# Performance work log

Measured on AMD Instinct MI355X. Metric: run time of the kernel, lower is better.

## Reference

```python
import jax, jax.numpy as jnp
import numpy as np

D_MODEL = 1024
N_HEADS = 16
D_K = D_MODEL // N_HEADS
SEQ = 2048
BATCH = 2
THETA = 10000.0


def apply_rope(x, positions, theta):
    # x: [..., h, s, d_k], positions: [s]
    d_k = x.shape[-1]
    inv_freq = 1.0 / (theta ** (jnp.arange(0, d_k, 2, dtype=jnp.float32) / d_k))  # [d_k/2]
    ang = positions.astype(jnp.float32)[:, None] * inv_freq[None, :]  # [s, d_k/2]
    cos, sin = jnp.cos(ang), jnp.sin(ang)
    xe, xo = x[..., 0::2], x[..., 1::2]
    re = xe * cos - xo * sin
    ro = xe * sin + xo * cos
    return jnp.stack([re, ro], axis=-1).reshape(x.shape)


def setup_inputs() -> dict:
    key = jax.random.key(0)
    ks = jax.random.split(key, 7)
    f = lambda k, s: jax.random.normal(k, s, dtype=jnp.float32)
    return {
        "Q": f(ks[0], (BATCH, SEQ, D_MODEL)),
        "K": f(ks[1], (BATCH, SEQ, D_MODEL)),
        "V": f(ks[2], (BATCH, SEQ, D_MODEL)),
        "w_q": f(ks[3], (D_MODEL, D_MODEL)) * 0.02,
        "w_k": f(ks[4], (D_MODEL, D_MODEL)) * 0.02,
        "w_v": f(ks[5], (D_MODEL, D_MODEL)) * 0.02,
        "w_o": f(ks[6], (D_MODEL, D_MODEL)) * 0.02,
        "mask": jnp.tril(jnp.ones((SEQ, SEQ), dtype=bool)),
        "token_positions": jnp.arange(SEQ, dtype=jnp.int32),
    }


def reference(Q, K, V, w_q, w_k, w_v, w_o, mask, token_positions):
    h, d_k = N_HEADS, D_K
    # projections: weight is [h*d_k, d_model], applied as x @ W^T
    def proj(x, w):
        y = jnp.einsum('bsd,ed->bse', x, w)
        b, s, _ = y.shape
        return y.reshape(b, s, h, d_k).transpose(0, 2, 1, 3)  # [b,h,s,d_k]
    q = proj(Q, w_q)
    k = proj(K, w_k)
    v = proj(V, w_v)
    q = apply_rope(q, token_positions, THETA)
    k = apply_rope(k, token_positions, THETA)
    scores = jnp.einsum('bhqd,bhkd->bhqk', q, k) / jnp.sqrt(jnp.float32(d_k))
    scores = jnp.where(mask, scores, -jnp.inf)
    attn = jax.nn.softmax(scores, axis=-1)
    out = jnp.einsum('bhqk,bhkd->bhqd', attn, v)
    b, _, s, _ = out.shape
    out = out.transpose(0, 2, 1, 3).reshape(b, s, h * d_k)
    return jnp.einsum('bse,de->bsd', out, w_o)
```

## Files before the change

kernel.cpp:

```cpp
#include <hip/hip_runtime.h>

#define SEQ 2048
#define BATCH 2
#define DM 1024
#define NH 16
#define DK 64
#define BH (BATCH*NH)

typedef __attribute__((ext_vector_type(8))) short bf16x8;
typedef __attribute__((ext_vector_type(4))) float f32x4;

__device__ __forceinline__ ushort f2bf(float f) {
  union { float f; unsigned u; } v; v.f = f;
  unsigned r = (v.u + 0x7fffu + ((v.u >> 16) & 1u)) >> 16;
  return (ushort)r;
}
__device__ __forceinline__ float bf2f(ushort h) {
  union { unsigned u; float f; } v; v.u = ((unsigned)h) << 16;
  return v.f;
}
__device__ __forceinline__ unsigned cvtpk(float lo, float hi) {
  unsigned r;
  asm("v_cvt_pk_bf16_f32 %0, %1, %2" : "=v"(r) : "v"(lo), "v"(hi));
  return r;
}

#define WAITV4 asm volatile("s_waitcnt vmcnt(4)" ::: "memory")
#define WAITV3 asm volatile("s_waitcnt vmcnt(3)" ::: "memory")
#define WAITV0 asm volatile("s_waitcnt vmcnt(0)" ::: "memory")
#define WAITL0 asm volatile("s_waitcnt lgkmcnt(0)" ::: "memory")
#define BARR() __builtin_amdgcn_s_barrier()

struct P4 { const float* p0; const float* p1; const float* p2; const float* p3; };
__global__ void k_castN(P4 in, ushort* __restrict__ out, int n4) {
  const float* src = (blockIdx.z == 0) ? in.p0 : (blockIdx.z == 1) ? in.p1
                    : (blockIdx.z == 2) ? in.p2 : in.p3;
  ushort* dst = out + (size_t)blockIdx.z * (size_t)n4 * 4;
  int i = blockIdx.x * blockDim.x + threadIdx.x;
  int st = gridDim.x * blockDim.x;
  for (; i < n4; i += st) {
    float4 v = reinterpret_cast<const float4*>(src)[i];
    ushort4 o;
    o.x = f2bf(v.x); o.y = f2bf(v.y); o.z = f2bf(v.z); o.w = f2bf(v.w);
    reinterpret_cast<ushort4*>(dst)[i] = o;
  }
}

__global__ void k_rope_tab(float* __restrict__ tab) {
  int id = blockIdx.x * blockDim.x + threadIdx.x;
  if (id >= SEQ * 32) return;
  int s = id >> 5, i = id & 31;
  float inv = powf(10000.f, -(float)i / 32.f);
  float ang = (float)s * inv;
  float sn, cs;
  sincosf(ang, &sn, &cs);
  tab[id * 2] = cs;
  tab[id * 2 + 1] = sn;
}

__global__ __launch_bounds__(256) void k_tr_v(const ushort* __restrict__ Y,
                                              ushort* __restrict__ VT) {
  __shared__ ushort tile[64][65];
  const int st = blockIdx.x, bh = blockIdx.y;
  const int b = bh >> 4, h = bh & 15;
  const int d = threadIdx.x & 63, s4 = threadIdx.x >> 6;
#pragma unroll
  for (int p = 0; p < 16; ++p) {
    int sl = p * 4 + s4;
    tile[d][sl] = Y[(size_t)(b * SEQ + st * 64 + sl) * DM + h * 64 + d];
  }
  __syncthreads();
  const int sl = threadIdx.x & 63, d4 = threadIdx.x >> 6;
#pragma unroll
  for (int p = 0; p < 16; ++p) {
    int dl = p * 4 + d4;
    VT[(size_t)bh * DK * SEQ + (size_t)dl * SEQ + st * 64 + sl] = tile[dl][sl];
  }
}

__device__ __forceinline__ void gll16(const void* g, void* l) {
  __builtin_amdgcn_global_load_lds((const __attribute__((address_space(1))) void*)g,
                                   (__attribute__((address_space(3))) void*)l, 16, 0, 0);
}

#define GSTAGE(AD, BD, kk_) do {                                               \
    gll16(A + (size_t)(m0 + w * 16 + lrow) * K + (kk_) + lcol, (void*)((AD) + w * 512));        \
    gll16(A + (size_t)(m0 + 64 + w * 16 + lrow) * K + (kk_) + lcol, (void*)((AD) + 2048 + w * 512)); \
    gll16(Bw + (size_t)(n0 + w * 16 + lrow) * K + (kk_) + lcol, (void*)((BD) + w * 512));       \
    gll16(Bw + (size_t)(n0 + 64 + w * 16 + lrow) * K + (kk_) + lcol, (void*)((BD) + 2048 + w * 512)); \
  } while (0)

#define GCOMP(AS_, BS_) do {                                                   \
    bf16x8 af[4], bfr[4];                                                      \
    _Pragma("unroll")                                                          \
    for (int i = 0; i < 4; ++i)                                                \
      af[i] = *(const bf16x8*)((AS_) + (wr * 64 + i * 16 + l15) * 32 + l4 * 8);\
    _Pragma("unroll")                                                          \
    for (int i = 0; i < 4; ++i)                                                \
      bfr[i] = *(const bf16x8*)((BS_) + (wc * 64 + i * 16 + l15) * 32 + l4 * 8);\
    _Pragma("unroll")                                                          \
    for (int mi = 0; mi < 4; ++mi)                                             \
      _Pragma("unroll")                                                        \
      for (int ni = 0; ni < 4; ++ni)                                           \
        acc[mi][ni] = __builtin_amdgcn_mfma_f32_16x16x32_bf16(af[mi], bfr[ni], acc[mi][ni], 0, 0, 0); \
  } while (0)

__global__ __launch_bounds__(256) void k_gemm_qkv(const ushort* __restrict__ A,
                                                  const ushort* __restrict__ Bw,
                                                  ushort* __restrict__ qT,
                                                  ushort* __restrict__ kT,
                                                  ushort* __restrict__ YV,
                                                  const float* __restrict__ tab,
                                                  float qscale, int M, int N, int K) {
  const int id = blockIdx.x;
  const int mlo = id & 7, nb = (id >> 3) & 7, mhi = (id >> 6) & 3, z = id >> 8;
  const int m0 = (mhi * 8 + mlo) * 128, n0 = nb * 128;
  A += (size_t)z * ((size_t)M * K);
  Bw += (size_t)z * ((size_t)N * K);
  __shared__ ushort As0[128 * 32], Bs0[128 * 32];
  __shared__ ushort As1[128 * 32], Bs1[128 * 32];
  const int tid = threadIdx.x;
  const int w = tid >> 6, lane = tid & 63;
  const int l15 = lane & 15, l4 = lane >> 4;
  const int wr = w >> 1, wc = w & 1;
  const int lrow = lane >> 2, lcol = (lane & 3) * 8;
  f32x4 acc[4][4] = {};
  GSTAGE(As0, Bs0, 0);
  GSTAGE(As1, Bs1, 32);
  for (int kk = 0; kk < K - 64; kk += 64) {
    WAITV4; BARR();
    GCOMP(As0, Bs0);
    WAITL0; BARR();
    GSTAGE(As0, Bs0, kk + 64);
    WAITV4; BARR();
    GCOMP(As1, Bs1);
    WAITL0; BARR();
    if (kk + 96 < K) GSTAGE(As1, Bs1, kk + 96);
  }
  WAITV4; BARR();
  GCOMP(As0, Bs0);
  WAITV0; BARR();
  GCOMP(As1, Bs1);
  if (z == 2) {
#pragma unroll
    for (int mi = 0; mi < 4; ++mi)
#pragma unroll
      for (int ni = 0; ni < 4; ++ni)
#pragma unroll
        for (int r = 0; r < 4; ++r) {
          int row = m0 + wr * 64 + mi * 16 + l4 * 4 + r;
          int col = n0 + wc * 64 + ni * 16 + l15;
          YV[(size_t)row * N + col] = f2bf(acc[mi][ni][r]);
        }
  } else {
    const float scale = (z == 0) ? qscale : 1.0f;
    ushort* T = (z == 0) ? qT : kT;
    const bool odd = (l15 & 1);
#pragma unroll
    for (int mi = 0; mi < 4; ++mi)
#pragma unroll
      for (int ni = 0; ni < 4; ++ni)
#pragma unroll
        for (int r = 0; r < 4; ++r) {
          int row = m0 + wr * 64 + mi * 16 + l4 * 4 + r;
          int col = n0 + wc * 64 + ni * 16 + l15;
          float v = acc[mi][ni][r];
          float pv = __shfl_xor(v, 1);
          int s = row & (SEQ - 1);
          int d = col & 63;
          float2 cs = *(const float2*)(tab + ((size_t)s * 32 + (d >> 1)) * 2);
          float xe = odd ? pv : v, xo = odd ? v : pv;
          float outv = (odd ? (xe * cs.y + xo * cs.x) : (xe * cs.x - xo * cs.y)) * scale;
          int bh = (row >> 11) * 16 + (col >> 6);
          T[((size_t)bh * SEQ + s) * 64 + d] = f2bf(outv);
        }
  }
}

#define FSTAGE(AD, BD, kk_) do {                                               \
    gll16(A + (size_t)(m0 + srow) * K + (kk_) + scol, (void*)((AD) + w * 512));\
    gll16(Bw + (size_t)(n0 + srow) * K + (kk_) + scol, (void*)((BD) + w * 512));\
    gll16(Bw + (size_t)(n0 + 64 + srow) * K + (kk_) + scol, (void*)((BD) + 2048 + w * 512)); \
  } while (0)

#define FCOMP(AS_, BS_) do {                                                   \
    bf16x8 af[2], bfr[4];                                                      \
    _Pragma("unroll")                                                          \
    for (int i = 0; i < 2; ++i)                                                \
      af[i] = *(const bf16x8*)((AS_) + (wr * 32 + i * 16 + l15) * 32 + l4 * 8);\
    _Pragma("unroll")                                                          \
    for (int i = 0; i < 4; ++i)                                                \
      bfr[i] = *(const bf16x8*)((BS_) + (wc * 64 + i * 16 + l15) * 32 + l4 * 8);\
    _Pragma("unroll")                                                          \
    for (int mi = 0; mi < 2; ++mi)                                             \
      _Pragma("unroll")                                                        \
      for (int ni = 0; ni < 4; ++ni)                                           \
        acc[mi][ni] = __builtin_amdgcn_mfma_f32_16x16x32_bf16(af[mi], bfr[ni], acc[mi][ni], 0, 0, 0); \
  } while (0)

__global__ __launch_bounds__(256) void k_gemm_f(const ushort* __restrict__ A,
                                                const ushort* __restrict__ Bw,
                                                float* __restrict__ C, int M, int N, int K) {
  const int id = blockIdx.x;
  const int mlo = id & 7, nb = (id >> 3) & 7, mhi = id >> 6;
  const int m0 = (mhi * 8 + mlo) * 64, n0 = nb * 128;
  __shared__ ushort As0[64 * 32], Bs0[128 * 32];
  __shared__ ushort As1[64 * 32], Bs1[128 * 32];
  const int tid = threadIdx.x;
  const int w = tid >> 6, lane = tid & 63;
  const int l15 = lane & 15, l4 = lane >> 4;
  const int wr = w >> 1, wc = w & 1;
  const int srow = tid >> 2, scol = (tid & 3) * 8;
  f32x4 acc[2][4] = {};
  FSTAGE(As0, Bs0, 0);
  FSTAGE(As1, Bs1, 32);
  for (int kk = 0; kk < K - 64; kk += 64) {
    WAITV3; BARR();
    FCOMP(As0, Bs0);
    WAITL0; BARR();
    FSTAGE(As0, Bs0, kk + 64);
    WAITV3; BARR();
    FCOMP(As1, Bs1);
    WAITL0; BARR();
    if (kk + 96 < K) FSTAGE(As1, Bs1, kk + 96);
  }
  WAITV3; BARR();
  FCOMP(As0, Bs0);
  WAITV0; BARR();
  FCOMP(As1, Bs1);
#pragma unroll
  for (int mi = 0; mi < 2; ++mi)
#pragma unroll
    for (int ni = 0; ni < 4; ++ni)
#pragma unroll
      for (int r = 0; r < 4; ++r) {
        int row = m0 + wr * 32 + mi * 16 + l4 * 4 + r;
        int col = n0 + wc * 64 + ni * 16 + l15;
        C[(size_t)row * N + col] = acc[mi][ni][r];
      }
}

#define STAGE1(DST, src, srcstride) do {                                       \
    _Pragma("unroll")                                                          \
    for (int i_ = 0; i_ < 2; ++i_) {                                           \
      int tt_ = i_ * 256 + tid;                                                \
      int row_ = tt_ >> 3, c_ = (tt_ & 7) ^ (row_ & 7);                        \
      gll16(src + (size_t)row_ * (srcstride) + c_ * 8,                         \
            (void*)((char*)(DST) + (i_ * 256 + w * 64) * 16));                 \
    }                                                                          \
  } while (0)

#define STAGE(KD, VD, kt_) do {                                                \
    const ushort* kb_ = kT + hb + (size_t)(kt_) * 4096;                        \
    const ushort* vb_ = vT + vbase + (size_t)(kt_) * 64;                       \
    STAGE1(KD, kb_, 64);                                                       \
    STAGE1(VD, vb_, SEQ);                                                      \
  } while (0)

#define LDSFRAG(BASE, row_, cidx)                                              \
  (*(const bf16x8*)((const char*)(BASE) + (row_) * 128 + (((cidx) ^ (l15 & 7)) * 16)))

#define SMAXUPD(P, MRUN, LRUN, SO) do {                                        \
    float a0 = fmaxf(fmaxf(P[0][0], P[0][1]), fmaxf(P[0][2], P[0][3]));        \
    float a1 = fmaxf(fmaxf(P[1][0], P[1][1]), fmaxf(P[1][2], P[1][3]));        \
    float a2 = fmaxf(fmaxf(P[2][0], P[2][1]), fmaxf(P[2][2], P[2][3]));        \
    float a3 = fmaxf(fmaxf(P[3][0], P[3][1]), fmaxf(P[3][2], P[3][3]));        \
    float mx = fmaxf(fmaxf(a0, a1), fmaxf(a2, a3));                            \
    mx = fmaxf(mx, __shfl_xor(mx, 16));                                        \
    mx = fmaxf(mx, __shfl_xor(mx, 32));                                        \
    const float mn = fmaxf(MRUN, mx);                                          \
    SO = __builtin_amdgcn_exp2f(MRUN - mn);                                    \
    float rs = 0.f;                                                            \
    _Pragma("unroll")                                                          \
    for (int nf = 0; nf < 4; ++nf) {                                           \
      float e0 = __builtin_amdgcn_exp2f(P[nf][0] - mn);                        \
      float e1 = __builtin_amdgcn_exp2f(P[nf][1] - mn);                        \
      float e2 = __builtin_amdgcn_exp2f(P[nf][2] - mn);                        \
      float e3 = __builtin_amdgcn_exp2f(P[nf][3] - mn);                        \
      P[nf][0] = e0; P[nf][1] = e1; P[nf][2] = e2; P[nf][3] = e3;              \
      rs += (e0 + e1) + (e2 + e3);                                             \
    }                                                                          \
    rs += __shfl_xor(rs, 16);                                                  \
    rs += __shfl_xor(rs, 32);                                                  \
    LRUN = LRUN * SO + rs;                                                     \
    MRUN = mn;                                                                 \
  } while (0)

#define RESCALE(ACC, SO) do {                                                  \
    float soq[4];                                                              \
    _Pragma("unroll")                                                          \
    for (int r = 0; r < 4; ++r) soq[r] = __shfl(SO, l4 * 4 + r);               \
    _Pragma("unroll")                                                          \
    for (int df = 0; df < 4; ++df)                                             \
      _Pragma("unroll")                                                        \
      for (int r = 0; r < 4; ++r) ACC[df][r] *= soq[r];                        \
  } while (0)

#define PWRITE(P, MYP) do {                                                    \
    _Pragma("unroll")                                                          \
    for (int nf = 0; nf < 4; ++nf) {                                           \
      uint2 pk;                                                                \
      pk.x = cvtpk(P[nf][0], P[nf][1]);                                        \
      pk.y = cvtpk(P[nf][2], P[nf][3]);                                        \
      *(uint2*)((MYP) + ((l15 * 128 + nf * 32 + l4 * 8) ^ swz)) = pk;          \
    }                                                                          \
  } while (0)

#define STEP2(KC, VC, KN, VN, kt_, M0, M1, PREF) do {                          \
    if (PREF) { STAGE(KN, VN, (kt_) + 1); }                                    \
    float p0[4][4], p1[4][4];                                                  \
    _Pragma("unroll")                                                          \
    for (int nf = 0; nf < 4; ++nf) {                                           \
      bf16x8 k0_ = LDSFRAG(KC, nf * 16 + l15, l4);                             \
      bf16x8 k1_ = LDSFRAG(KC, nf * 16 + l15, l4 + 4);                         \
      if (M0 >= 0) {                                                           \
        f32x4 z = {0.f, 0.f, 0.f, 0.f};                                        \
        z = __builtin_amdgcn_mfma_f32_16x16x32_bf16(k0_, qb00, z, 0, 0, 0);    \
        z = __builtin_amdgcn_mfma_f32_16x16x32_bf16(k1_, qb01, z, 0, 0, 0);    \
        _Pragma("unroll")                                                      \
        for (int r = 0; r < 4; ++r) {                                          \
          float sc = z[r];                                                     \
          if (M0 == 1 && (nf * 16 + l4 * 4 + r) > (w * 16 + l15)) sc = -INFINITY; \
          p0[nf][r] = sc;                                                      \
        }                                                                      \
      }                                                                        \
      {                                                                        \
        f32x4 z = {0.f, 0.f, 0.f, 0.f};                                        \
        z = __builtin_amdgcn_mfma_f32_16x16x32_bf16(k0_, qb10, z, 0, 0, 0);    \
        z = __builtin_amdgcn_mfma_f32_16x16x32_bf16(k1_, qb11, z, 0, 0, 0);    \
        _Pragma("unroll")                                                      \
        for (int r = 0; r < 4; ++r) {                                          \
          float sc = z[r];                                                     \
          if (M1 == 1 && (nf * 16 + l4 * 4 + r) > (w * 16 + l15)) sc = -INFINITY; \
          p1[nf][r] = sc;                                                      \
        }                                                                      \
      }                                                                        \
    }                                                                          \
    float so0_, so1_;                                                          \
    if (M0 >= 0) { SMAXUPD(p0, mrun0, lrun0, so0_); RESCALE(acc0, so0_); PWRITE(p0, myP0); } \
    SMAXUPD(p1, mrun1, lrun1, so1_); RESCALE(acc1, so1_); PWRITE(p1, myP1);    \
    bf16x8 pa00, pa01, pa10, pa11;                                             \
    if (M0 >= 0) {                                                             \
      pa00 = *(const bf16x8*)(myP0 + ((l15 * 128 + l4 * 16) ^ swz));           \
      pa01 = *(const bf16x8*)(myP0 + ((l15 * 128 + 64 + l4 * 16) ^ swz));      \
    }                                                                          \
    pa10 = *(const bf16x8*)(myP1 + ((l15 * 128 + l4 * 16) ^ swz));             \
    pa11 = *(const bf16x8*)(myP1 + ((l15 * 128 + 64 + l4 * 16) ^ swz));        \
    _Pragma("unroll")                                                          \
    for (int df = 0; df < 4; ++df) {                                           \
      bf16x8 v0_ = LDSFRAG(VC, df * 16 + l15, l4);                             \
      bf16x8 v1_ = LDSFRAG(VC, df * 16 + l15, l4 + 4);                         \
      if (M0 >= 0) {                                                           \
        acc0[df] = __builtin_amdgcn_mfma_f32_16x16x32_bf16(pa00, v0_, acc0[df], 0, 0, 0); \
        acc0[df] = __builtin_amdgcn_mfma_f32_16x16x32_bf16(pa01, v1_, acc0[df], 0, 0, 0); \
      }                                                                        \
      acc1[df] = __builtin_amdgcn_mfma_f32_16x16x32_bf16(pa10, v0_, acc1[df], 0, 0, 0); \
      acc1[df] = __builtin_amdgcn_mfma_f32_16x16x32_bf16(pa11, v1_, acc1[df], 0, 0, 0); \
    }                                                                          \
    __syncthreads();                                                           \
  } while (0)

__global__ __launch_bounds__(256, 3) void k_flash(const ushort* __restrict__ qT,
                                                  const ushort* __restrict__ kT,
                                                  const ushort* __restrict__ vT,
                                                  ushort* __restrict__ AO) {
  __shared__ ushort Ks[2][64 * 64];
  __shared__ ushort Vs[2][64 * 64];
  __shared__ char Plds[4 * 4096];
  const int l = blockIdx.x;
  const int bh = (l & 7) * 4 + ((l >> 3) & 3);
  const int qt = (SEQ / 128 - 1) - (l >> 5);
  const int tid = threadIdx.x, w = tid >> 6, lane = tid & 63;
  const int l15 = lane & 15, l4 = lane >> 4;
  const size_t hb = (size_t)bh * SEQ * DK;
  const size_t vbase = (size_t)bh * DK * SEQ;
  const int qrow0 = qt * 128 + w * 16;
  const int qrow1 = qrow0 + 64;
  const bf16x8 qb00 = *(const bf16x8*)(qT + hb + (size_t)(qrow0 + l15) * 64 + l4 * 8);
  const bf16x8 qb01 = *(const bf16x8*)(qT + hb + (size_t)(qrow0 + l15) * 64 + 32 + l4 * 8);
  const bf16x8 qb10 = *(const bf16x8*)(qT + hb + (size_t)(qrow1 + l15) * 64 + l4 * 8);
  const bf16x8 qb11 = *(const bf16x8*)(qT + hb + (size_t)(qrow1 + l15) * 64 + 32 + l4 * 8);
  f32x4 acc0[4] = {}, acc1[4] = {};
  float mrun0 = -INFINITY, lrun0 = 0.f, mrun1 = -INFINITY, lrun1 = 0.f;
  char* myP0 = (char*)Plds + w * 4096;
  char* myP1 = myP0 + 2048;
  const int swz = (l15 & 7) << 4;
  ushort* kc = &Ks[0][0]; ushort* vc = &Vs[0][0];
  ushort* kn = &Ks[1][0]; ushort* vn = &Vs[1][0];
  STAGE(kc, vc, 0);
  __syncthreads();
  for (int kt = 0; kt < 2 * qt; ++kt) {
    STEP2(kc, vc, kn, vn, kt, 0, 0, true);
    ushort* t;
    t = kc; kc = kn; kn = t;
    t = vc; vc = vn; vn = t;
  }
  STEP2(kc, vc, kn, vn, 2 * qt, 1, 0, true);
  {
    ushort* t;
    t = kc; kc = kn; kn = t;
    t = vc; vc = vn; vn = t;
  }
  STEP2(kc, vc, kn, vn, 2 * qt + 1, -1, 1, false);
  const int b = bh >> 4, h = bh & 15;
  float lq0[4], lq1[4];
#pragma unroll
  for (int r = 0; r < 4; ++r) {
    lq0[r] = __shfl(lrun0, l4 * 4 + r);
    lq1[r] = __shfl(lrun1, l4 * 4 + r);
  }
#pragma unroll
  for (int r = 0; r < 4; ++r) {
    float inv0 = 1.f / lq0[r], inv1 = 1.f / lq1[r];
    int qr0 = qrow0 + l4 * 4 + r, qr1 = qrow1 + l4 * 4 + r;
#pragma unroll
    for (int df = 0; df < 4; ++df) {
      AO[(size_t)(b * SEQ + qr0) * DM + h * 64 + df * 16 + l15] = f2bf(acc0[df][r] * inv0);
      AO[(size_t)(b * SEQ + qr1) * DM + h * 64 + df * 16 + l15] = f2bf(acc1[df][r] * inv1);
    }
  }
}

extern "C" void kernel_launch(void* const* d_in, const int* in_sizes, int n_in,
                              void* d_out, int out_size, void* d_ws, size_t ws_size,
                              hipStream_t stream) {
  const float* Q = (const float*)d_in[0];
  const float* K = (const float*)d_in[1];
  const float* V = (const float*)d_in[2];
  const float* wq = (const float*)d_in[3];
  const float* wk = (const float*)d_in[4];
  const float* wv = (const float*)d_in[5];
  const float* wo = (const float*)d_in[6];
  float* out = (float*)d_out;
  char* ws = (char*)d_ws;

  ushort* XQ = (ushort*)(ws + 0);
  ushort* XK = (ushort*)(ws + 8388608);
  ushort* WQ = (ushort*)(ws + 25165824);
  ushort* qT = (ushort*)(ws + 33554432);
  ushort* kT = (ushort*)(ws + 41943040);
  ushort* YV = (ushort*)(ws + 50331648);
  float* TAB = (float*)(ws + 58720256);
  ushort* vT = XQ;
  ushort* AO = XK;

  const int NX4 = BATCH * SEQ * DM / 4;
  const int NW4 = DM * DM / 4;
  P4 xin = {Q, K, V, nullptr};
  P4 win = {wq, wk, wv, wo};
  k_castN<<<dim3(1024, 1, 3), 256, 0, stream>>>(xin, XQ, NX4);
  k_castN<<<dim3(1024, 1, 4), 256, 0, stream>>>(win, WQ, NW4);
  k_rope_tab<<<(SEQ * 32) / 256, 256, 0, stream>>>(TAB);

  const float QSCALE = 0.125f * 1.4426950408889634f;
  k_gemm_qkv<<<768, 256, 0, stream>>>(XQ, WQ, qT, kT, YV, TAB, QSCALE,
                                      BATCH * SEQ, DM, DM);

  k_tr_v<<<dim3(SEQ / 64, BH), 256, 0, stream>>>(YV, vT);

  k_flash<<<BH * (SEQ / 128), 256, 0, stream>>>(qT, kT, vT, AO);

  k_gemm_f<<<512, 256, 0, stream>>>(AO, WQ + 3 * DM * DM, out, BATCH * SEQ, DM, DM);
}
```

Baseline: 130.2 us.

## Widen flash-attention KV tile to 128 keys with conditional rescale

Doubles the key/value tile per iteration from 64 to 128 rows, which halves the loop trip count and the number of barriers and softmax reductions. The online-softmax rescale of the accumulators is now skipped whenever the running max does not increase. The row-sum cross-lane reduction is deferred to the end. The larger LDS buffers force occupancy down from 3 to 2 blocks per CU, and register pressure rises from the 8x4 score arrays.

```diff
diff --git a/kernel.cpp b/kernel.cpp
--- a/kernel.cpp
+++ b/kernel.cpp
@@ -240,89 +240,106 @@
       }
 }
 
-#define STAGE1(DST, src, srcstride) do {                                       \
-    _Pragma("unroll")                                                          \
-    for (int i_ = 0; i_ < 2; ++i_) {                                           \
+#define KSTAGE(DST, kt_) do {                                                  \
+    const ushort* kb_ = kT + hb + (size_t)(kt_) * 8192;                        \
+    _Pragma("unroll")                                                          \
+    for (int i_ = 0; i_ < 4; ++i_) {                                           \
       int tt_ = i_ * 256 + tid;                                                \
       int row_ = tt_ >> 3, c_ = (tt_ & 7) ^ (row_ & 7);                        \
-      gll16(src + (size_t)row_ * (srcstride) + c_ * 8,                         \
+      gll16(kb_ + (size_t)row_ * 64 + c_ * 8,                                  \
             (void*)((char*)(DST) + (i_ * 256 + w * 64) * 16));                 \
     }                                                                          \
   } while (0)
 
-#define STAGE(KD, VD, kt_) do {                                                \
-    const ushort* kb_ = kT + hb + (size_t)(kt_) * 4096;                        \
-    const ushort* vb_ = vT + vbase + (size_t)(kt_) * 64;                       \
-    STAGE1(KD, kb_, 64);                                                       \
-    STAGE1(VD, vb_, SEQ);                                                      \
-  } while (0)
-
-#define LDSFRAG(BASE, row_, cidx)                                              \
-  (*(const bf16x8*)((const char*)(BASE) + (row_) * 128 + (((cidx) ^ (l15 & 7)) * 16)))
-
-#define SMAXUPD(P, MRUN, LRUN, SO) do {                                        \
-    float a0 = fmaxf(fmaxf(P[0][0], P[0][1]), fmaxf(P[0][2], P[0][3]));        \
-    float a1 = fmaxf(fmaxf(P[1][0], P[1][1]), fmaxf(P[1][2], P[1][3]));        \
-    float a2 = fmaxf(fmaxf(P[2][0], P[2][1]), fmaxf(P[2][2], P[2][3]));        \
-    float a3 = fmaxf(fmaxf(P[3][0], P[3][1]), fmaxf(P[3][2], P[3][3]));        \
-    float mx = fmaxf(fmaxf(a0, a1), fmaxf(a2, a3));                            \
+#define VSTAGE(DST, kt_) do {                                                  \
+    const ushort* vb_ = vT + vbase + (size_t)(kt_) * 128;                      \
+    _Pragma("unroll")                                                          \
+    for (int i_ = 0; i_ < 4; ++i_) {                                           \
+      int tt_ = i_ * 256 + tid;                                                \
+      int row_ = tt_ >> 4, c_ = (tt_ & 15) ^ (row_ & 15);                      \
+      gll16(vb_ + (size_t)row_ * SEQ + c_ * 8,                                 \
+            (void*)((char*)(DST) + (i_ * 256 + w * 64) * 16));                 \
+    }                                                                          \
+  } while (0)
+
+#define FRK(BASE, row_, cidx)                                                  \
+  (*(const bf16x8*)((const char*)(BASE) + (row_) * 128 + ((((cidx) ^ ((row_) & 7)) & 7) * 16)))
+#define FRV(BASE, row_, cidx)                                                  \
+  (*(const bf16x8*)((const char*)(BASE) + (row_) * 256 + ((((cidx) ^ ((row_) & 15)) & 15) * 16)))
+
+#define SMAX8(P, MRUN, LRUN, ACC) do {                                         \
+    float mx = P[0][0];                                                        \
+    _Pragma("unroll")                                                          \
+    for (int nf = 0; nf < 8; ++nf)                                             \
+      _Pragma("unroll")                                                        \
+      for (int r = 0; r < 4; ++r) mx = fmaxf(mx, P[nf][r]);                    \
     mx = fmaxf(mx, __shfl_xor(mx, 16));                                        \
     mx = fmaxf(mx, __shfl_xor(mx, 32));                                        \
-    const float mn = fmaxf(MRUN, mx);                                          \
-    SO = __builtin_amdgcn_exp2f(MRUN - mn);                                    \
+    if (!__all(mx <= MRUN)) {                                                  \
+      const float mn = fmaxf(MRUN, mx);                                        \
+      const float so = __builtin_amdgcn_exp2f(MRUN - mn);                      \
+      float soq[4];                                                            \
+      _Pragma("unroll")                                                        \
+      for (int r = 0; r < 4; ++r) soq[r] = __shfl(so, l4 * 4 + r);             \
+      _Pragma("unroll")                                                        \
+      for (int df = 0; df < 4; ++df)                                           \
+        _Pragma("unroll")                                                      \
+        for (int r = 0; r < 4; ++r) ACC[df][r] *= soq[r];                      \
+      LRUN *= so;                                                              \
+      MRUN = mn;                                                               \
+    }                                                                          \
     float rs = 0.f;                                                            \
     _Pragma("unroll")                                                          \
-    for (int nf = 0; nf < 4; ++nf) {                                           \
-      float e0 = __builtin_amdgcn_exp2f(P[nf][0] - mn);                        \
-      float e1 = __builtin_amdgcn_exp2f(P[nf][1] - mn);                        \
-      float e2 = __builtin_amdgcn_exp2f(P[nf][2] - mn);                        \
-      float e3 = __builtin_amdgcn_exp2f(P[nf][3] - mn);                        \
+    for (int nf = 0; nf < 8; ++nf) {                                           \
+      float e0 = __builtin_amdgcn_exp2f(P[nf][0] - MRUN);                      \
+      float e1 = __builtin_amdgcn_exp2f(P[nf][1] - MRUN);                      \
+      float e2 = __builtin_amdgcn_exp2f(P[nf][2] - MRUN);                      \
+      float e3 = __builtin_amdgcn_exp2f(P[nf][3] - MRUN);                      \
       P[nf][0] = e0; P[nf][1] = e1; P[nf][2] = e2; P[nf][3] = e3;              \
       rs += (e0 + e1) + (e2 + e3);                                             \
     }                                                                          \
-    rs += __shfl_xor(rs, 16);                                                  \
-    rs += __shfl_xor(rs, 32);                                                  \
-    LRUN = LRUN * SO + rs;                                                     \
-    MRUN = mn;                                                                 \
-  } while (0)
-
-#define RESCALE(ACC, SO) do {                                                  \
-    float soq[4];                                                              \
-    _Pragma("unroll")                                                          \
-    for (int r = 0; r < 4; ++r) soq[r] = __shfl(SO, l4 * 4 + r);               \
-    _Pragma("unroll")                                                          \
-    for (int df = 0; df < 4; ++df)                                             \
-      _Pragma("unroll")                                                        \
-      for (int r = 0; r < 4; ++r) ACC[df][r] *= soq[r];                        \
-  } while (0)
-
-#define PWRITE(P, MYP) do {                                                    \
-    _Pragma("unroll")                                                          \
-    for (int nf = 0; nf < 4; ++nf) {                                           \
+    LRUN += rs;                                                                \
+  } while (0)
+
+#define PVHALF(P, MYP, ACC, VC, H) do {                                        \
+    _Pragma("unroll")                                                          \
+    for (int i = 0; i < 4; ++i) {                                              \
       uint2 pk;                                                                \
-      pk.x = cvtpk(P[nf][0], P[nf][1]);                                        \
-      pk.y = cvtpk(P[nf][2], P[nf][3]);                                        \
-      *(uint2*)((MYP) + ((l15 * 128 + nf * 32 + l4 * 8) ^ swz)) = pk;          \
-    }                                                                          \
-  } while (0)
-
-#define STEP2(KC, VC, KN, VN, kt_, M0, M1, PREF) do {                          \
-    if (PREF) { STAGE(KN, VN, (kt_) + 1); }                                    \
-    float p0[4][4], p1[4][4];                                                  \
-    _Pragma("unroll")                                                          \
-    for (int nf = 0; nf < 4; ++nf) {                                           \
-      bf16x8 k0_ = LDSFRAG(KC, nf * 16 + l15, l4);                             \
-      bf16x8 k1_ = LDSFRAG(KC, nf * 16 + l15, l4 + 4);                         \
-      if (M0 >= 0) {                                                           \
+      pk.x = cvtpk(P[(H) * 4 + i][0], P[(H) * 4 + i][1]);                      \
+      pk.y = cvtpk(P[(H) * 4 + i][2], P[(H) * 4 + i][3]);                      \
+      *(uint2*)((MYP) + ((l15 * 128 + i * 32 + l4 * 8) ^ swz)) = pk;           \
+    }                                                                          \
+    const bf16x8 pa0 = *(const bf16x8*)((MYP) + ((l15 * 128 + l4 * 16) ^ swz));\
+    const bf16x8 pa1 = *(const bf16x8*)((MYP) + ((l15 * 128 + 64 + l4 * 16) ^ swz));\
+    _Pragma("unroll")                                                          \
+    for (int df = 0; df < 4; ++df) {                                           \
+      bf16x8 v0_ = FRV(VC, df * 16 + l15, (H) * 8 + l4);                       \
+      bf16x8 v1_ = FRV(VC, df * 16 + l15, (H) * 8 + l4 + 4);                   \
+      ACC[df] = __builtin_amdgcn_mfma_f32_16x16x32_bf16(pa0, v0_, ACC[df], 0, 0, 0); \
+      ACC[df] = __builtin_amdgcn_mfma_f32_16x16x32_bf16(pa1, v1_, ACC[df], 0, 0, 0); \
+    }                                                                          \
+  } while (0)
+
+#define STEP(KC, VC, KN, VN, kt_, DIAG, PREF) do {                             \
+    if (PREF) { KSTAGE(KN, (kt_) + 1); VSTAGE(VN, (kt_) + 1); }                \
+    float p0[8][4], p1[8][4];                                                  \
+    _Pragma("unroll")                                                          \
+    for (int nf = 0; nf < 8; ++nf) {                                           \
+      bf16x8 k0_ = FRK(KC, nf * 16 + l15, l4);                                 \
+      bf16x8 k1_ = FRK(KC, nf * 16 + l15, l4 + 4);                             \
+      if (!(DIAG) || nf < 4) {                                                 \
         f32x4 z = {0.f, 0.f, 0.f, 0.f};                                        \
         z = __builtin_amdgcn_mfma_f32_16x16x32_bf16(k0_, qb00, z, 0, 0, 0);    \
         z = __builtin_amdgcn_mfma_f32_16x16x32_bf16(k1_, qb01, z, 0, 0, 0);    \
         _Pragma("unroll")                                                      \
         for (int r = 0; r < 4; ++r) {                                          \
           float sc = z[r];                                                     \
-          if (M0 == 1 && (nf * 16 + l4 * 4 + r) > (w * 16 + l15)) sc = -INFINITY; \
+          if (DIAG && (nf * 16 + l4 * 4 + r) > (w * 16 + l15)) sc = -INFINITY; \
           p0[nf][r] = sc;                                                      \
         }                                                                      \
+      } else {                                                                 \
+        _Pragma("unroll")                                                      \
+        for (int r = 0; r < 4; ++r) p0[nf][r] = -INFINITY;                     \
       }                                                                        \
       {                                                                        \
         f32x4 z = {0.f, 0.f, 0.f, 0.f};                                        \
@@ -331,41 +348,26 @@
         _Pragma("unroll")                                                      \
         for (int r = 0; r < 4; ++r) {                                          \
           float sc = z[r];                                                     \
-          if (M1 == 1 && (nf * 16 + l4 * 4 + r) > (w * 16 + l15)) sc = -INFINITY; \
+          if (DIAG && (nf * 16 + l4 * 4 + r) > (64 + w * 16 + l15)) sc = -INFINITY; \
           p1[nf][r] = sc;                                                      \
         }                                                                      \
       }                                                                        \
     }                                                                          \
-    float so0_, so1_;                                                          \
-    if (M0 >= 0) { SMAXUPD(p0, mrun0, lrun0, so0_); RESCALE(acc0, so0_); PWRITE(p0, myP0); } \
-    SMAXUPD(p1, mrun1, lrun1, so1_); RESCALE(acc1, so1_); PWRITE(p1, myP1);    \
-    bf16x8 pa00, pa01, pa10, pa11;                                             \
-    if (M0 >= 0) {                                                             \
-      pa00 = *(const bf16x8*)(myP0 + ((l15 * 128 + l4 * 16) ^ swz));           \
-      pa01 = *(const bf16x8*)(myP0 + ((l15 * 128 + 64 + l4 * 16) ^ swz));      \
-    }                                                                          \
-    pa10 = *(const bf16x8*)(myP1 + ((l15 * 128 + l4 * 16) ^ swz));             \
-    pa11 = *(const bf16x8*)(myP1 + ((l15 * 128 + 64 + l4 * 16) ^ swz));        \
-    _Pragma("unroll")                                                          \
-    for (int df = 0; df < 4; ++df) {                                           \
-      bf16x8 v0_ = LDSFRAG(VC, df * 16 + l15, l4);                             \
-      bf16x8 v1_ = LDSFRAG(VC, df * 16 + l15, l4 + 4);                         \
-      if (M0 >= 0) {                                                           \
-        acc0[df] = __builtin_amdgcn_mfma_f32_16x16x32_bf16(pa00, v0_, acc0[df], 0, 0, 0); \
-        acc0[df] = __builtin_amdgcn_mfma_f32_16x16x32_bf16(pa01, v1_, acc0[df], 0, 0, 0); \
-      }                                                                        \
-      acc1[df] = __builtin_amdgcn_mfma_f32_16x16x32_bf16(pa10, v0_, acc1[df], 0, 0, 0); \
-      acc1[df] = __builtin_amdgcn_mfma_f32_16x16x32_bf16(pa11, v1_, acc1[df], 0, 0, 0); \
-    }                                                                          \
+    SMAX8(p0, mrun0, lrun0, acc0);                                             \
+    SMAX8(p1, mrun1, lrun1, acc1);                                             \
+    PVHALF(p0, myP0, acc0, VC, 0);                                             \
+    if (!(DIAG)) PVHALF(p0, myP0, acc0, VC, 1);                                \
+    PVHALF(p1, myP1, acc1, VC, 0);                                             \
+    PVHALF(p1, myP1, acc1, VC, 1);                                             \
     __syncthreads();                                                           \
   } while (0)
 
-__global__ __launch_bounds__(256, 3) void k_flash(const ushort* __restrict__ qT,
+__global__ __launch_bounds__(256, 2) void k_flash(const ushort* __restrict__ qT,
                                                   const ushort* __restrict__ kT,
                                                   const ushort* __restrict__ vT,
                                                   ushort* __restrict__ AO) {
-  __shared__ ushort Ks[2][64 * 64];
-  __shared__ ushort Vs[2][64 * 64];
+  __shared__ ushort Ks[2][128 * 64];
+  __shared__ ushort Vs[2][64 * 128];
   __shared__ char Plds[4 * 4096];
   const int l = blockIdx.x;
   const int bh = (l & 7) * 4 + ((l >> 3) & 3);
@@ -387,21 +389,17 @@
   const int swz = (l15 & 7) << 4;
   ushort* kc = &Ks[0][0]; ushort* vc = &Vs[0][0];
   ushort* kn = &Ks[1][0]; ushort* vn = &Vs[1][0];
-  STAGE(kc, vc, 0);
+  KSTAGE(kc, 0); VSTAGE(vc, 0);
   __syncthreads();
-  for (int kt = 0; kt < 2 * qt; ++kt) {
-    STEP2(kc, vc, kn, vn, kt, 0, 0, true);
+  for (int kt = 0; kt < qt; ++kt) {
+    STEP(kc, vc, kn, vn, kt, false, true);
     ushort* t;
     t = kc; kc = kn; kn = t;
     t = vc; vc = vn; vn = t;
   }
-  STEP2(kc, vc, kn, vn, 2 * qt, 1, 0, true);
-  {
-    ushort* t;
-    t = kc; kc = kn; kn = t;
-    t = vc; vc = vn; vn = t;
-  }
-  STEP2(kc, vc, kn, vn, 2 * qt + 1, -1, 1, false);
+  STEP(kc, vc, kn, vn, qt, true, false);
+  lrun0 += __shfl_xor(lrun0, 16); lrun0 += __shfl_xor(lrun0, 32);
+  lrun1 += __shfl_xor(lrun1, 16); lrun1 += __shfl_xor(lrun1, 32);
   const int b = bh >> 4, h = bh & 15;
   float lq0[4], lq1[4];
 #pragma unroll
```

After: 127.0 us. 1.03x faster.
